# Kernel optimization log

Measured on AMD Instinct MI355X. Metric: run time of the kernel, lower is better.

The kernel has to match this reference:

```python
import jax, jax.numpy as jnp
import numpy as np

CONF_TH = 0.9
FRACTION = 0.66
IGNORE = 255
LAMBDA = 1.0


def _image_mask(max_prob, lab, num_classes):
    """max_prob: [N] float, lab: [N] int32 pseudo labels. Returns [N] bool mask.

    Faithful to the torch loop: per class c, keep the top int(count_c * FRACTION)
    pixels of that class by confidence, OR any pixel with confidence > CONF_TH.
    Implemented with ONE sort per image + within-class cumulative rank.
    """
    N = max_prob.shape[0]
    mask_prob = max_prob > CONF_TH
    # per-class pixel counts and top-k budget (int() truncates in torch)
    counts = jnp.zeros((num_classes,), jnp.int32).at[lab].add(1)
    k = (counts.astype(jnp.float32) * FRACTION).astype(jnp.int32)
    # sort pixels by confidence descending (stable; no ties with random floats)
    order = jnp.argsort(-max_prob)
    lab_s = lab[order]
    # within-class rank in sorted order: rank 0 = most confident pixel of its class
    onehot = jax.nn.one_hot(lab_s, num_classes, dtype=jnp.int32)  # [N, C]
    rank = jnp.take_along_axis(jnp.cumsum(onehot, axis=0), lab_s[:, None], axis=1)[:, 0] - 1
    sel_s = rank < k[lab_s]
    mask_topk = jnp.zeros((N,), bool).at[order].set(sel_s)
    return mask_prob | mask_topk


def setup_inputs() -> dict:
    key = jax.random.key(0)
    pred = jax.random.normal(key, (8, 19, 512, 1024), dtype=jnp.float32)
    return {"pred": pred}


def reference(pred):
    B, C, H, W = pred.shape
    N = H * W
    # teacher is None -> pseudo labels from pred itself (detached)
    pred_sg = jax.lax.stop_gradient(pred)
    prob = jax.nn.softmax(pred_sg, axis=1)
    max_prob = prob.max(axis=1).reshape(B, N)          # [B, N]
    lab = jnp.argmax(pred_sg, axis=1).astype(jnp.int32).reshape(B, N)  # [B, N]
    mask = jax.vmap(lambda mp, l: _image_mask(mp, l, C))(max_prob, lab)  # [B, N] bool
    pseudo = jnp.where(mask, lab, IGNORE)
    # cross-entropy with ignore_index, mean over kept pixels
    logp = jax.nn.log_softmax(pred, axis=1)            # [B, C, H, W]
    logp = logp.transpose(0, 2, 3, 1).reshape(B, N, C)  # [B, N, C]
    valid = pseudo != IGNORE
    tgt = jnp.where(valid, pseudo, 0)
    nll = -jnp.take_along_axis(logp, tgt[:, :, None], axis=2)[:, :, 0]  # [B, N]
    denom = jnp.maximum(jnp.sum(valid), 1).astype(pred.dtype)
    loss = jnp.sum(nll * valid.astype(pred.dtype)) / denom
    return loss * LAMBDA
```

## Files before the change

kernel.cpp:

```cpp
#include <hip/hip_runtime.h>
#include <stdint.h>

#define BLK 256

constexpr int Bsz = 8, Ccls = 19, Hh = 512, Ww = 1024;
constexpr int Npix = Hh * Ww;
constexpr int TotPix = Bsz * Npix;
constexpr int NGroup = Bsz * Ccls;
constexpr int SUBS = 128;
constexpr int NB1 = 256;
constexpr int NB2 = 4096;
constexpr int KEY_BASE = 122 << 5;

__device__ __forceinline__ int key1_of(uint32_t u) {
  int k = (int)(u >> 18) - KEY_BASE;
  return k < 0 ? 0 : (k > 255 ? 255 : k);
}

__global__ __launch_bounds__(BLK) void k_fused(const float* __restrict__ pred,
                                               float4* __restrict__ mp_out,
                                               uchar4* __restrict__ lab_out,
                                               uint32_t* __restrict__ h1) {
  __shared__ uint32_t hist[Ccls * NB1];
  int t = threadIdx.x;
#pragma unroll
  for (int c = 0; c < Ccls; ++c) hist[c * NB1 + t] = 0;
  __syncthreads();

  int blk = blockIdx.x;
  int b = blk >> 7;
  int s = blk & 127;
  const float* ibase = pred + (size_t)b * Ccls * Npix;
  int n0 = s * 4096;

  for (int j = 0; j < 4; ++j) {
    int n = n0 + j * 1024 + t * 4;
    float4 v0 = *(const float4*)(ibase + n);
    float m[4] = {v0.x, v0.y, v0.z, v0.w};
    float sm[4] = {1.f, 1.f, 1.f, 1.f};
    int lc[4] = {0, 0, 0, 0};
    for (int cb = 1; cb < Ccls; cb += 6) {
      float4 vv[6];
#pragma unroll
      for (int i = 0; i < 6; ++i)
        vv[i] = *(const float4*)(ibase + (size_t)(cb + i) * Npix + n);
#pragma unroll
      for (int i = 0; i < 6; ++i) {
        int c = cb + i;
        const float* vf = (const float*)&vv[i];
#pragma unroll
        for (int q = 0; q < 4; ++q) {
          float x = vf[q];
          bool gt = x > m[q];
          float mn = gt ? x : m[q];
          sm[q] = sm[q] * __expf(m[q] - mn) + __expf(x - mn);
          m[q] = mn;
          lc[q] = gt ? c : lc[q];
        }
      }
    }
    float mp[4];
#pragma unroll
    for (int q = 0; q < 4; ++q) {
      mp[q] = 1.0f / sm[q];
      atomicAdd(&hist[lc[q] * NB1 + key1_of(__float_as_uint(mp[q]))], 1u);
    }
    int p4 = b * (Npix / 4) + (n >> 2);
    mp_out[p4] = make_float4(mp[0], mp[1], mp[2], mp[3]);
    lab_out[p4] = make_uchar4((uint8_t)lc[0], (uint8_t)lc[1], (uint8_t)lc[2], (uint8_t)lc[3]);
  }

  __syncthreads();
  uint32_t* dst = h1 + (size_t)blk * (Ccls * NB1);
#pragma unroll
  for (int c = 0; c < Ccls; ++c) dst[c * NB1 + t] = hist[c * NB1 + t];
}

__global__ __launch_bounds__(BLK) void k_select1(const uint32_t* __restrict__ h1,
                                                 int* __restrict__ selhi,
                                                 int* __restrict__ rem) {
  int g = blockIdx.x;
  int b = g / Ccls, c = g % Ccls;
  int t = threadIdx.x;
  int bin = NB1 - 1 - t;
  uint32_t cnt = 0;
  for (int s = 0; s < SUBS; ++s)
    cnt += h1[(size_t)(b * SUBS + s) * (Ccls * NB1) + c * NB1 + bin];
  __shared__ uint32_t sc[BLK];
  sc[t] = cnt;
  __syncthreads();
  for (int ofs = 1; ofs < BLK; ofs <<= 1) {
    uint32_t vv = (t >= ofs) ? sc[t - ofs] : 0u;
    __syncthreads();
    sc[t] += vv;
    __syncthreads();
  }
  uint32_t incl = sc[t];
  uint32_t excl = incl - cnt;
  uint32_t total = sc[BLK - 1];
  int k = (int)((float)total * 0.66f);
  if (t == 0 && k == 0) { selhi[g] = -1; rem[g] = 0; }
  if (k > 0 && (int)excl < k && k <= (int)incl) {
    selhi[g] = bin;
    rem[g] = k - (int)excl;
  }
}

__global__ __launch_bounds__(BLK) void k_hist2(const float4* __restrict__ mp,
                                               const uchar4* __restrict__ lab,
                                               const int* __restrict__ selhi,
                                               uint32_t* __restrict__ hist2) {
  int p4 = blockIdx.x * BLK + threadIdx.x;
  int b = p4 >> 17;
  float4 m = mp[p4];
  uchar4 l = lab[p4];
  const float* mf = (const float*)&m;
  const uint8_t* lf = (const uint8_t*)&l;
#pragma unroll
  for (int q = 0; q < 4; ++q) {
    uint32_t u = __float_as_uint(mf[q]);
    int g = b * Ccls + (int)lf[q];
    if (key1_of(u) == selhi[g])
      atomicAdd(&hist2[g * NB2 + (int)((u >> 6) & 0xFFFu)], 1u);
  }
}

__global__ __launch_bounds__(BLK) void k_select2(const uint32_t* __restrict__ hist2,
                                                 const int* __restrict__ selhi,
                                                 const int* __restrict__ rem,
                                                 uint32_t* __restrict__ thresh) {
  int g = blockIdx.x;
  int t = threadIdx.x;
  int sh = selhi[g];
  if (sh < 0) { if (t == 0) thresh[g] = 0x7F800000u; return; }
  const uint32_t* h = hist2 + g * NB2;
  uint32_t loc[16]; uint32_t psum = 0;
  int hi = NB2 - 1 - t * 16;
#pragma unroll
  for (int i = 0; i < 16; ++i) { loc[i] = h[hi - i]; psum += loc[i]; }
  __shared__ uint32_t sc[BLK];
  sc[t] = psum;
  __syncthreads();
  for (int ofs = 1; ofs < BLK; ofs <<= 1) {
    uint32_t vv = (t >= ofs) ? sc[t - ofs] : 0u;
    __syncthreads();
    sc[t] += vv;
    __syncthreads();
  }
  uint32_t incl = sc[t];
  int k = rem[g];
  uint32_t excl = incl - psum;
  if (k > 0 && (int)excl < k && k <= (int)incl) {
    uint32_t cum = excl;
#pragma unroll
    for (int i = 0; i < 16; ++i) {
      if ((uint32_t)k <= cum + loc[i]) {
        thresh[g] = ((uint32_t)(sh + KEY_BASE) << 18) | ((uint32_t)(hi - i) << 6);
        break;
      }
      cum += loc[i];
    }
  }
}

__global__ __launch_bounds__(BLK) void k_loss(const float4* __restrict__ mp_arr,
                                              const uchar4* __restrict__ lab,
                                              const uint32_t* __restrict__ thresh,
                                              float* __restrict__ gsum,
                                              uint32_t* __restrict__ gcnt,
                                              uint32_t* __restrict__ ticket,
                                              float* __restrict__ out) {
  int p4 = blockIdx.x * BLK + threadIdx.x;
  int b = p4 >> 17;
  float4 m = mp_arr[p4];
  uchar4 l = lab[p4];
  const float* mf = (const float*)&m;
  const uint8_t* lf = (const uint8_t*)&l;
  float vs = 0.f; uint32_t vc = 0u;
#pragma unroll
  for (int q = 0; q < 4; ++q) {
    float mp = mf[q];
    int g = b * Ccls + (int)lf[q];
    uint32_t u = __float_as_uint(mp);
    bool sel = (mp > 0.9f) || (u >= thresh[g]);
    if (sel) { vs += -logf(mp); vc += 1u; }
  }
#pragma unroll
  for (int o = 32; o > 0; o >>= 1) {
    vs += __shfl_down(vs, o, 64);
    vc += __shfl_down(vc, o, 64);
  }
  __shared__ float ssum[BLK / 64];
  __shared__ uint32_t scnt[BLK / 64];
  int wave = threadIdx.x >> 6;
  int lane = threadIdx.x & 63;
  if (lane == 0) { ssum[wave] = vs; scnt[wave] = vc; }
  __syncthreads();
  if (threadIdx.x == 0) {
    float ts = 0.f; uint32_t tc = 0u;
#pragma unroll
    for (int w = 0; w < BLK / 64; ++w) { ts += ssum[w]; tc += scnt[w]; }
    atomicAdd(gsum, ts);
    atomicAdd(gcnt, tc);
    __threadfence();
    uint32_t done = atomicAdd(ticket, 1u);
    if (done == gridDim.x - 1) {
      float fs = atomicAdd(gsum, 0.0f);
      uint32_t fc = atomicAdd(gcnt, 0u);
      out[0] = fs / (float)(fc > 0u ? fc : 1u);
    }
  }
}

extern "C" void kernel_launch(void* const* d_in, const int* in_sizes, int n_in,
                              void* d_out, int out_size, void* d_ws, size_t ws_size,
                              hipStream_t stream) {
  const float* pred = (const float*)d_in[0];
  char* ws = (char*)d_ws;
  size_t off = 0;
  auto carve = [&](size_t bytes) -> void* {
    void* p = ws + off;
    off = (off + bytes + 255) & ~(size_t)255;
    return p;
  };
  float*    mp    = (float*)carve((size_t)TotPix * 4);
  uint8_t*  lab   = (uint8_t*)carve((size_t)TotPix);
  uint32_t* h1    = (uint32_t*)carve((size_t)Bsz * SUBS * Ccls * NB1 * 4);
  int*      selhi = (int*)carve((size_t)NGroup * 4);
  int*      rem   = (int*)carve((size_t)NGroup * 4);
  uint32_t* thr   = (uint32_t*)carve((size_t)NGroup * 4);
  size_t zero_off = off;
  uint32_t* hist2 = (uint32_t*)carve((size_t)NGroup * NB2 * 4);
  float*    gsum  = (float*)carve(4);
  uint32_t* gcnt  = (uint32_t*)carve(4);
  uint32_t* tick  = (uint32_t*)carve(4);

  hipMemsetAsync(ws + zero_off, 0, off - zero_off, stream);

  int nblk4 = TotPix / (BLK * 4);
  k_fused  <<<Bsz * SUBS, BLK, 0, stream>>>(pred, (float4*)mp, (uchar4*)lab, h1);
  k_select1<<<NGroup,     BLK, 0, stream>>>(h1, selhi, rem);
  k_hist2  <<<nblk4,      BLK, 0, stream>>>((const float4*)mp, (const uchar4*)lab, selhi, hist2);
  k_select2<<<NGroup,     BLK, 0, stream>>>(hist2, selhi, rem, thr);
  k_loss   <<<nblk4,      BLK, 0, stream>>>((const float4*)mp, (const uchar4*)lab, thr,
                                            gsum, gcnt, tick, (float*)d_out);
}
```

Before: 536.4 us.

## Stage class logits through LDS via async global_load_lds and two-pass softmax

The fused softmax/argmax kernel now copies each 256-pixel tile of all 19 class planes into shared memory using the direct global-to-LDS load builtin. Each thread then computes one pixel with a two-pass max-then-exp tree reduction instead of an online softmax over four pixels. The aim is to cut dependent online-softmax exp chains and raise ILP. The cost is a barrier per tile with no double buffering, so loads and compute do not overlap, plus scalar rather than vectorised output stores.

```diff
diff --git a/kernel.cpp b/kernel.cpp
--- a/kernel.cpp
+++ b/kernel.cpp
@@ -11,16 +11,25 @@
 constexpr int NB1 = 256;
 constexpr int NB2 = 4096;
 constexpr int KEY_BASE = 122 << 5;
+constexpr int TILE = 256;
+constexpr int TILES_PER_BLK = 16;
 
 __device__ __forceinline__ int key1_of(uint32_t u) {
   int k = (int)(u >> 18) - KEY_BASE;
   return k < 0 ? 0 : (k > 255 ? 255 : k);
 }
 
+__device__ __forceinline__ void load_lds16(const float* g, float* l) {
+  __builtin_amdgcn_global_load_lds(
+      (const __attribute__((address_space(1))) uint32_t*)g,
+      (__attribute__((address_space(3))) uint32_t*)l, 16, 0, 0);
+}
+
 __global__ __launch_bounds__(BLK) void k_fused(const float* __restrict__ pred,
-                                               float4* __restrict__ mp_out,
-                                               uchar4* __restrict__ lab_out,
+                                               float* __restrict__ mp_out,
+                                               uint8_t* __restrict__ lab_out,
                                                uint32_t* __restrict__ h1) {
+  __shared__ float tile[Ccls * TILE];
   __shared__ uint32_t hist[Ccls * NB1];
   int t = threadIdx.x;
 #pragma unroll
@@ -31,46 +40,51 @@
   int b = blk >> 7;
   int s = blk & 127;
   const float* ibase = pred + (size_t)b * Ccls * Npix;
-  int n0 = s * 4096;
-
-  for (int j = 0; j < 4; ++j) {
-    int n = n0 + j * 1024 + t * 4;
-    float4 v0 = *(const float4*)(ibase + n);
-    float m[4] = {v0.x, v0.y, v0.z, v0.w};
-    float sm[4] = {1.f, 1.f, 1.f, 1.f};
-    int lc[4] = {0, 0, 0, 0};
-    for (int cb = 1; cb < Ccls; cb += 6) {
-      float4 vv[6];
-#pragma unroll
-      for (int i = 0; i < 6; ++i)
-        vv[i] = *(const float4*)(ibase + (size_t)(cb + i) * Npix + n);
-#pragma unroll
-      for (int i = 0; i < 6; ++i) {
-        int c = cb + i;
-        const float* vf = (const float*)&vv[i];
-#pragma unroll
-        for (int q = 0; q < 4; ++q) {
-          float x = vf[q];
-          bool gt = x > m[q];
-          float mn = gt ? x : m[q];
-          sm[q] = sm[q] * __expf(m[q] - mn) + __expf(x - mn);
-          m[q] = mn;
-          lc[q] = gt ? c : lc[q];
-        }
-      }
-    }
-    float mp[4];
-#pragma unroll
-    for (int q = 0; q < 4; ++q) {
-      mp[q] = 1.0f / sm[q];
-      atomicAdd(&hist[lc[q] * NB1 + key1_of(__float_as_uint(mp[q]))], 1u);
-    }
-    int p4 = b * (Npix / 4) + (n >> 2);
-    mp_out[p4] = make_float4(mp[0], mp[1], mp[2], mp[3]);
-    lab_out[p4] = make_uchar4((uint8_t)lc[0], (uint8_t)lc[1], (uint8_t)lc[2], (uint8_t)lc[3]);
-  }
-
-  __syncthreads();
+  int wave = t >> 6, lane = t & 63;
+
+  for (int j = 0; j < TILES_PER_BLK; ++j) {
+    int n = s * 4096 + j * TILE;
+    for (int c = wave; c < Ccls; c += 4)
+      load_lds16(ibase + (size_t)c * Npix + n + lane * 4, &tile[c * TILE + lane * 4]);
+    __syncthreads();
+
+    float v[Ccls];
+#pragma unroll
+    for (int c = 0; c < Ccls; ++c) v[c] = tile[c * TILE + t];
+
+    float m8[10];
+#pragma unroll
+    for (int i = 0; i < 9; ++i) m8[i] = fmaxf(v[2 * i], v[2 * i + 1]);
+    m8[9] = v[18];
+    float m4[5];
+#pragma unroll
+    for (int i = 0; i < 5; ++i) m4[i] = fmaxf(m8[2 * i], m8[2 * i + 1]);
+    float m = fmaxf(fmaxf(fmaxf(m4[0], m4[1]), fmaxf(m4[2], m4[3])), m4[4]);
+
+    int lc = 18;
+#pragma unroll
+    for (int c = 17; c >= 0; --c) lc = (v[c] == m) ? c : lc;
+
+    float e[Ccls];
+#pragma unroll
+    for (int c = 0; c < Ccls; ++c) e[c] = __expf(v[c] - m);
+    float s8[10];
+#pragma unroll
+    for (int i = 0; i < 9; ++i) s8[i] = e[2 * i] + e[2 * i + 1];
+    s8[9] = e[18];
+    float s4[5];
+#pragma unroll
+    for (int i = 0; i < 5; ++i) s4[i] = s8[2 * i] + s8[2 * i + 1];
+    float sum = (s4[0] + s4[1]) + (s4[2] + s4[3]) + s4[4];
+    float mp = 1.0f / sum;
+
+    atomicAdd(&hist[lc * NB1 + key1_of(__float_as_uint(mp))], 1u);
+    int p = b * Npix + n + t;
+    mp_out[p] = mp;
+    lab_out[p] = (uint8_t)lc;
+    __syncthreads();
+  }
+
   uint32_t* dst = h1 + (size_t)blk * (Ccls * NB1);
 #pragma unroll
   for (int c = 0; c < Ccls; ++c) dst[c * NB1 + t] = hist[c * NB1 + t];
@@ -238,7 +252,7 @@
   hipMemsetAsync(ws + zero_off, 0, off - zero_off, stream);
 
   int nblk4 = TotPix / (BLK * 4);
-  k_fused  <<<Bsz * SUBS, BLK, 0, stream>>>(pred, (float4*)mp, (uchar4*)lab, h1);
+  k_fused  <<<Bsz * SUBS, BLK, 0, stream>>>(pred, mp, lab, h1);
   k_select1<<<NGroup,     BLK, 0, stream>>>(h1, selhi, rem);
   k_hist2  <<<nblk4,      BLK, 0, stream>>>((const float4*)mp, (const uchar4*)lab, selhi, hist2);
   k_select2<<<NGroup,     BLK, 0, stream>>>(hist2, selhi, rem, thr);
```

Result: no change. 542.7 us (+1.2%).
